# Performance work log

Hardware: AMD Instinct MI355X
Metric: run time of the kernel (lower is better)

The kernel has to match this reference:

```python
import jax, jax.numpy as jnp
from jax import lax
import numpy as np

NUM_COEFF = 24      # solver.num_coeff_per_dim (Chebyshev coefficients)
NUM_POINTS = 48     # Chebyshev-Gauss collocation nodes per interval
PICARD_ITERS = 5    # fixed-point iterations of the spectral PAN solve


def _cheb_setup(dtype):
    j = jnp.arange(NUM_POINTS, dtype=dtype)
    n = jnp.arange(NUM_COEFF, dtype=dtype)
    # tau_j = cos(pi*(j+1/2)/P); T[n, j] = T_n(tau_j) = cos(n*arccos(tau_j))
    ang = jnp.pi * (j + 0.5) / NUM_POINTS
    T = jnp.cos(n[:, None] * ang[None, :])                  # [C, P]
    V = (2.0 / NUM_POINTS) * T
    V = V.at[0].mul(0.5)                                    # DCT: a_n = sum_j f(tau_j) V[n, j]
    signs = jnp.cos(n * jnp.pi)                             # T_n(-1) = (-1)^n
    return T, V, signs


def _cheb_antiderivative(a, signs):
    # Chebyshev coeffs of int_{-1}^{tau} f, given coeffs a of f: b_n = (a_{n-1}-a_{n+1})/(2n)
    C = a.shape[-1]
    a_pad = jnp.concatenate([a, jnp.zeros_like(a[..., :2])], axis=-1)
    n = jnp.arange(1, C, dtype=a.dtype)
    b_rest = (a_pad[..., 0:C - 1] - a_pad[..., 2:C + 1]) / (2.0 * n)
    b0 = -jnp.sum(b_rest * signs[1:], axis=-1, keepdims=True)  # enforce value 0 at tau=-1
    return jnp.concatenate([b0, b_rest], axis=-1)


def _vf(y, W1, b1, W2, b2):
    # neural vector field f(t, y): autonomous MLP
    return jnp.tanh(y @ W1 + b1) @ W2 + b2


def _pan_solve(y_init, t_span, W1, b1, W2, b2):
    # Chebyshev-spectral (PAN) ODE solve; returns trajectory at t_span points
    # and the per-interval coefficient tensors B_all [I, batch, dim, C]
    T, V, signs = _cheb_setup(y_init.dtype)

    def solve_interval(y0, ts):
        t0, t1 = ts[0], ts[1]
        scale = (t1 - t0) * 0.5                             # dtau -> dt Jacobian

        def picard(B, _):
            y_nodes = jnp.einsum('bdc,cp->pbd', B, T)       # y at collocation nodes
            fvals = _vf(y_nodes, W1, b1, W2, b2)            # [P, batch, dim]
            a = jnp.einsum('pbd,cp->bdc', fvals, V)         # Chebyshev coeffs of f
            Bn = scale * _cheb_antiderivative(a, signs)
            Bn = Bn.at[..., 0].add(y0)                      # y(tau=-1) = y0
            return Bn, None

        B0 = jnp.zeros((*y0.shape, NUM_COEFF), y0.dtype).at[..., 0].set(y0)
        B, _ = lax.scan(picard, B0, None, length=PICARD_ITERS)
        y1 = jnp.sum(B, axis=-1)                            # T_n(1) = 1
        return y1, (B, y1)

    ts = jnp.stack([t_span[:-1], t_span[1:]], axis=-1)      # [I, 2]
    _, (B_all, y_ends) = lax.scan(solve_interval, y_init, ts)
    traj = jnp.concatenate([y_init[None], y_ends], axis=0)  # [I+1, batch, dim]
    return traj, B_all


def setup_inputs() -> dict:
    key = jax.random.key(0)
    k1, k2, k3 = jax.random.split(key, 3)
    batch, dim, hidden = 256, 512, 512
    s = np.float32(1.0 / np.sqrt(dim))
    return {
        'y_init': jax.random.normal(k1, (batch, dim), jnp.float32),
        't_span': jnp.linspace(0.0, 1.0, 7, dtype=jnp.float32),
        'W1': s * jax.random.normal(k2, (dim, hidden), jnp.float32),
        'b1': jnp.zeros((hidden,), jnp.float32),
        'W2': s * jax.random.normal(k3, (hidden, dim), jnp.float32),
        'b2': jnp.zeros((dim,), jnp.float32),
    }


def reference(y_init, t_span, W1, b1, W2, b2):
    traj, _B_all = _pan_solve(y_init, t_span, W1, b1, W2, b2)
    return (t_span, traj)
```

## Files before the change

### kernel.cpp

```cpp
#include <hip/hip_runtime.h>
#include <hip/hip_bf16.h>
#include <math.h>

#define NC 24
#define NP 48
#define NI 6
#define BATCH 256
#define DIM 512
#define NELEM (BATCH*DIM)
#define PROWS (BATCH*NC)

typedef __bf16 bf16x8 __attribute__((ext_vector_type(8)));
typedef unsigned short u16x8 __attribute__((ext_vector_type(8)));
typedef float f32x4 __attribute__((ext_vector_type(4)));
using bf16 = __hip_bfloat16;

struct bq8 { __hip_bfloat162 a, b; };

__device__ __forceinline__ void gld_lds16(const void* g, void* l) {
  __builtin_amdgcn_global_load_lds(
      (const __attribute__((address_space(1))) void*)g,
      (__attribute__((address_space(3))) void*)l, 16, 0, 0);
}

__device__ __forceinline__ float fast_tanh(float x) {
  float u = __expf(2.0f * x);
  float r = __builtin_amdgcn_rcpf(u + 1.0f);
  return __builtin_fmaf(-2.0f, r, 1.0f);
}

__device__ __forceinline__ float bfu(unsigned short u) {
  union { unsigned int i; float f; } v; v.i = ((unsigned)u) << 16; return v.f;
}

__global__ __launch_bounds__(256) void k_prep1(
    const float* __restrict__ t_span, const float* __restrict__ W1,
    const float* __restrict__ W2, const float* __restrict__ b1,
    const float* __restrict__ b2, const float* __restrict__ y_init,
    bf16* __restrict__ Tbf, bf16* __restrict__ Abf, float* __restrict__ a1,
    float* __restrict__ rs, float* __restrict__ wv, float* __restrict__ scales,
    float* __restrict__ zbias, float* __restrict__ out,
    bf16* __restrict__ W1T, bf16* __restrict__ W2T, bf16* __restrict__ W2bf,
    float* __restrict__ bb, float* __restrict__ y0, bf16* __restrict__ y0bf) {
  int bid = blockIdx.x;
  int tid = threadIdx.x;
  if (bid < 1024) {
    int idx = bid*256 + tid;
    int k = idx >> 9, n = idx & 511;
    W1T[n*DIM + k] = __float2bfloat16(W1[idx]);
    W2T[n*DIM + k] = __float2bfloat16(W2[idx]);
    W2bf[idx]      = __float2bfloat16(W2[idx]);
  } else if (bid < 1536) {
    int i = (bid - 1024)*256 + tid;
    float v = y_init[i];
    y0[i] = v; out[7 + i] = v;
    y0bf[i] = __float2bfloat16(v);
  } else if (bid < 1538) {
    int h = (bid - 1536)*256 + tid;
    float s = 0.f;
    for (int d = 0; d < DIM; d++) s = fmaf(b2[d], W1[d*DIM + h], s);
    bb[h] = s;
  } else {
    __shared__ double Tsh[NC][NP];
    __shared__ double Ashd[NC][NP];
    __shared__ double a1sh[NC];
    __shared__ double wsh[NP];
    for (int idx = tid; idx < NC*NP; idx += 256) {
      int c = idx / NP, p = idx % NP;
      Tsh[c][p] = cos((double)c * (M_PI * ((double)p + 0.5) / NP));
    }
    for (int idx = tid; idx < 32*64; idx += 256) Abf[idx] = __float2bfloat16(0.f);
    for (int idx = tid; idx < 48*32; idx += 256) Tbf[idx] = __float2bfloat16(0.f);
    __syncthreads();
    if (tid < NP) {
      int q = tid;
      double V[NC], K[NC];
      for (int c = 0; c < NC; c++) V[c] = (2.0/NP) * Tsh[c][q];
      V[0] *= 0.5;
      double s = 0.0;
      for (int n = 1; n < NC; n++) {
        double hi = (n+1 < NC) ? V[n+1] : 0.0;
        K[n] = (V[n-1] - hi) / (2.0*n);
        s += (n & 1) ? -K[n] : K[n];
      }
      K[0] = -s;
      double wsum = 0.0;
      for (int c = 0; c < NC; c++) wsum += K[c];
      wv[q] = (float)wsum;
      wsh[q] = wsum;
      for (int c = 0; c < NC; c++) {
        Ashd[c][q] = K[c];
        Abf[c*64 + q] = __float2bfloat16((float)K[c]);
      }
    }
    __syncthreads();
    if (tid < NC) {
      double s = 0.0;
      for (int q = 0; q < NP; q++) s += Ashd[tid][q];
      a1sh[tid] = s;
      a1[tid] = (float)s;
    }
    __syncthreads();
    if (tid < NP) {
      int p = tid;
      double r = 0.0;
      for (int c = 0; c < NC; c++) r += Tsh[c][p] * a1sh[c];
      rs[p] = (float)r;
      for (int c = 0; c < NC; c++) Tbf[p*32 + c] = __float2bfloat16((float)Tsh[c][p]);
    }
    if (tid == 0) {
      double s = 0.0;
      for (int q = 0; q < NP; q++) s += wsh[q];
      scales[6] = (float)s;
    }
    for (int idx = tid; idx < DIM; idx += 256) zbias[idx] = 0.f;
    if (tid < NI) scales[tid] = 0.5f*(t_span[tid+1]-t_span[tid]);
    if (tid < NI+1) out[tid] = t_span[tid];
  }
}

template<int EPI>
__device__ __forceinline__ void gemm_body(int vbid, int vgrid,
    bf16 (*sA)[128*64], bf16 (*sB)[64*64],
    const bf16* __restrict__ A, const bf16* __restrict__ BT,
    const float* __restrict__ bias, bf16* __restrict__ outb,
    float* __restrict__ outf) {
  int tid = threadIdx.x;
  int lane = tid & 63, wid = tid >> 6;
  int q8 = vgrid >> 3;
  int tl = (vbid & 7)*q8 + (vbid >> 3);
  int bm = tl >> 3, bn = tl & 7;
  int row0 = bm*128, col0 = bn*64;
  int wr = wid >> 1, wc = wid & 1;
  int r16 = lane & 15, g = lane >> 4;

  f32x4 acc[4][2];
  #pragma unroll
  for (int m = 0; m < 4; m++)
    #pragma unroll
    for (int n = 0; n < 2; n++)
      acc[m][n] = {0.f, 0.f, 0.f, 0.f};

  auto stage = [&](int buf, int k0) {
    #pragma unroll
    for (int j = 0; j < 4; j++) {
      int cid = wid*64 + lane + j*256;
      int r = cid >> 3;
      int c = (cid & 7) ^ (r & 7);
      gld_lds16(A + (size_t)(row0 + r)*DIM + k0 + c*8,
                (char*)&sA[buf][0] + wid*1024 + j*4096);
    }
    #pragma unroll
    for (int j = 0; j < 2; j++) {
      int cid = wid*64 + lane + j*256;
      int r = cid >> 3;
      int c = (cid & 7) ^ (r & 7);
      gld_lds16(BT + (size_t)(col0 + r)*DIM + k0 + c*8,
                (char*)&sB[buf][0] + wid*1024 + j*4096);
    }
  };

  stage(0, 0);
  int cur = 0;
  for (int k0 = 0; k0 < DIM; k0 += 64) {
    if (k0 + 64 < DIM) {
      stage(cur ^ 1, k0 + 64);
      asm volatile("s_waitcnt vmcnt(6)" ::: "memory");
    } else {
      asm volatile("s_waitcnt vmcnt(0)" ::: "memory");
    }
    __builtin_amdgcn_s_barrier();
    #pragma unroll
    for (int kk = 0; kk < 2; kk++) {
      bf16x8 af[4], bfr[2];
      #pragma unroll
      for (int m = 0; m < 4; m++) {
        int r = wr*64 + m*16 + r16;
        af[m] = *(const bf16x8*)(&sA[cur][0] + r*64 + (((kk*4+g) ^ (r&7))*8));
      }
      #pragma unroll
      for (int n = 0; n < 2; n++) {
        int r = wc*32 + n*16 + r16;
        bfr[n] = *(const bf16x8*)(&sB[cur][0] + r*64 + (((kk*4+g) ^ (r&7))*8));
      }
      #pragma unroll
      for (int m = 0; m < 4; m++)
        #pragma unroll
        for (int n = 0; n < 2; n++)
          acc[m][n] = __builtin_amdgcn_mfma_f32_16x16x32_bf16(af[m], bfr[n], acc[m][n], 0, 0, 0);
    }
    __builtin_amdgcn_s_barrier();
    cur ^= 1;
  }

  #pragma unroll
  for (int m = 0; m < 4; m++) {
    int rowb = row0 + wr*64 + m*16 + g*4;
    #pragma unroll
    for (int n = 0; n < 2; n++) {
      int col = col0 + wc*32 + n*16 + r16;
      float bv = bias[col];
      #pragma unroll
      for (int r = 0; r < 4; r++) {
        float v = acc[m][n][r] + bv;
        size_t idx = (size_t)(rowb + r)*DIM + col;
        if constexpr (EPI == 1) {
          outb[idx] = __float2bfloat16(v);
        } else {
          outf[idx] = v;
          outb[idx] = __float2bfloat16(fast_tanh(v));
        }
      }
    }
  }
}

__global__ __launch_bounds__(256, 3) void k_prep2(
    const bf16* __restrict__ W1T, const bf16* __restrict__ W2bf,
    const float* __restrict__ zbias, bf16* __restrict__ W21T,
    const bf16* __restrict__ y0bf, const float* __restrict__ b1,
    bf16* __restrict__ H1, float* __restrict__ C) {
  __shared__ bf16 sA[2][128*64];
  __shared__ bf16 sB[2][64*64];
  if (blockIdx.x < 32)
    gemm_body<1>(blockIdx.x, 32, sA, sB, W1T, W2bf, zbias, W21T, nullptr);
  else
    gemm_body<2>(blockIdx.x - 32, 16, sA, sB, y0bf, W1T, b1, H1, C);
}

template<int MODE>
__global__ __launch_bounds__(256, 2) void k_iter(
    const bf16* __restrict__ Pin, const bf16* __restrict__ H1,
    const bf16* __restrict__ W21T, const float* __restrict__ Cg,
    const float* __restrict__ bbg, const bf16* __restrict__ Tbf,
    const bf16* __restrict__ Abf, const float* __restrict__ a1,
    const float* __restrict__ rsg, const float* __restrict__ wvg,
    const float* __restrict__ scales, int t, bf16* __restrict__ outp) {
  __shared__ char smem[49152];
  int tid = threadIdx.x;
  int lane = tid & 63, wid = tid >> 6;
  int r16 = lane & 15, g = lane >> 4;
  int q8 = gridDim.x >> 3;
  int tl = (blockIdx.x & 7)*q8 + (blockIdx.x >> 3);
  int bm = tl >> 2, bn = tl & 3;
  int col0 = bn*128;
  int bglob0 = bm*2;

  if constexpr (MODE != 0) {
    int row0 = bm*48;
    f32x4 acc[3][2];
    #pragma unroll
    for (int m = 0; m < 3; m++)
      #pragma unroll
      for (int n = 0; n < 2; n++)
        acc[m][n] = {0.f, 0.f, 0.f, 0.f};

    auto stage = [&](int buf, int k0) {
      #pragma unroll
      for (int j = 0; j < 2; j++) {
        if (lane < 48) {
          int cid = j*192 + wid*48 + lane;
          int r = cid >> 3, cc = (cid & 7) ^ (r & 7);
          gld_lds16(Pin + (size_t)(row0 + r)*DIM + k0 + cc*8,
                    smem + buf*6144 + j*3072 + wid*768);
        }
      }
      #pragma unroll
      for (int j = 0; j < 4; j++) {
        int cid = j*256 + wid*64 + lane;
        int r = cid >> 3, cc = (cid & 7) ^ (r & 7);
        gld_lds16(W21T + (size_t)(col0 + r)*DIM + k0 + cc*8,
                  smem + 12288 + buf*16384 + j*4096 + wid*1024);
      }
    };

    stage(0, 0);
    int cur = 0;
    for (int ks = 0; ks < 8; ks++) {
      if (ks < 7) {
        stage(cur ^ 1, (ks+1)*64);
        asm volatile("s_waitcnt vmcnt(6)" ::: "memory");
      } else {
        asm volatile("s_waitcnt vmcnt(0)" ::: "memory");
      }
      __builtin_amdgcn_s_barrier();
      const char* sAc = smem + cur*6144;
      const char* sBc = smem + 12288 + cur*16384;
      #pragma unroll
      for (int kk = 0; kk < 2; kk++) {
        bf16x8 af[3], bfr[2];
        #pragma unroll
        for (int m = 0; m < 3; m++) {
          int r = m*16 + r16;
          af[m] = *(const bf16x8*)(sAc + r*128 + ((kk*4+g) ^ (r&7))*16);
        }
        #pragma unroll
        for (int n = 0; n < 2; n++) {
          int r = wid*32 + n*16 + r16;
          bfr[n] = *(const bf16x8*)(sBc + r*128 + ((kk*4+g) ^ (r&7))*16);
        }
        #pragma unroll
        for (int m = 0; m < 3; m++)
          #pragma unroll
          for (int n = 0; n < 2; n++)
            acc[m][n] = __builtin_amdgcn_mfma_f32_16x16x32_bf16(af[m], bfr[n], acc[m][n], 0, 0, 0);
      }
      __builtin_amdgcn_s_barrier();
      cur ^= 1;
    }

    #pragma unroll
    for (int m = 0; m < 3; m++) {
      int rowf = m*16 + g*4;
      int b_loc = rowf >= 24 ? 1 : 0;
      int c0 = rowf - b_loc*24;
      int slot = c0 >> 3;
      int inb  = (c0*2) & 15;
      #pragma unroll
      for (int n = 0; n < 2; n++) {
        int h = wid*32 + n*16 + r16;
        char* ad = smem + b_loc*8192 + h*64 + (((slot ^ ((h>>1)&3)) << 4) | inb);
        bq8 v;
        v.a = __hip_bfloat162{__float2bfloat16(acc[m][n][0]), __float2bfloat16(acc[m][n][1])};
        v.b = __hip_bfloat162{__float2bfloat16(acc[m][n][2]), __float2bfloat16(acc[m][n][3])};
        *(bq8*)ad = v;
      }
    }
  } else {
    bf16* sH1 = (bf16*)(smem + 16384);
    #pragma unroll
    for (int j = 0; j < 4; j++) {
      int e = j*256 + tid;
      int b = e >> 9, k = e & 511;
      sH1[e] = H1[(size_t)(bglob0 + b)*DIM + k];
    }
    __syncthreads();
    int b = tid >> 7, hl = tid & 127;
    int hg = col0 + hl;
    const bf16* wrow = W21T + (size_t)hg*DIM;
    const bf16* hrow = sH1 + b*512;
    float g1 = 0.f;
    for (int ks = 0; ks < 64; ks++) {
      u16x8 w8 = *(const u16x8*)(wrow + ks*8);
      u16x8 h8 = *(const u16x8*)(hrow + ks*8);
      #pragma unroll
      for (int i = 0; i < 8; i++)
        g1 = fmaf(bfu(h8[i]), bfu(w8[i]), g1);
    }
    __syncthreads();
    int rot = ((hl>>1)&3) << 4;
    #pragma unroll
    for (int c = 0; c < NC; c++) {
      int lb = c*2;
      char* ad = smem + b*8192 + hl*64 + ((( (lb>>4) << 4) ^ rot) | (lb & 15));
      *(bf16*)ad = __float2bfloat16(a1[c]*g1);
    }
  }

  if (tid < 256) {
    int bz = tid >> 7, hz = tid & 127;
    *(f32x4*)(smem + bz*8192 + hz*64 + ((3 ^ ((hz>>1)&3)) << 4)) = f32x4{0.f,0.f,0.f,0.f};
  }
  __syncthreads();

  int b_w = wid >> 1;
  int h0 = (wid & 1) << 6;
  int bglob = bglob0 + b_w;
  float sc = scales[t];

  f32x4 acc2[3][4];
  #pragma unroll
  for (int pt = 0; pt < 3; pt++)
    #pragma unroll
    for (int n2 = 0; n2 < 4; n2++)
      acc2[pt][n2] = {0.f, 0.f, 0.f, 0.f};
  {
    bf16x8 afT[3];
    #pragma unroll
    for (int pt = 0; pt < 3; pt++)
      afT[pt] = *(const bf16x8*)(Tbf + (pt*16 + r16)*32 + g*8);
    #pragma unroll
    for (int n2 = 0; n2 < 4; n2++) {
      int h = h0 + n2*16 + r16;
      bf16x8 b8 = *(const bf16x8*)(smem + b_w*8192 + h*64 + ((g ^ ((h>>1)&3)) << 4));
      #pragma unroll
      for (int pt = 0; pt < 3; pt++)
        acc2[pt][n2] = __builtin_amdgcn_mfma_f32_16x16x32_bf16(afT[pt], b8, acc2[pt][n2], 0, 0, 0);
    }
  }

  float rsv[12];
  #pragma unroll
  for (int pt = 0; pt < 3; pt++)
    #pragma unroll
    for (int r = 0; r < 4; r++)
      rsv[pt*4+r] = rsg[pt*16 + g*4 + r];

  if constexpr (MODE == 2) {
    float wvv[12];
    #pragma unroll
    for (int pt = 0; pt < 3; pt++)
      #pragma unroll
      for (int r = 0; r < 4; r++)
        wvv[pt*4+r] = wvg[pt*16 + g*4 + r];
    #pragma unroll
    for (int n2 = 0; n2 < 4; n2++) {
      int hg2 = col0 + h0 + n2*16 + r16;
      float cv = Cg[(size_t)bglob*DIM + hg2];
      float bbv = bbg[hg2];
      float hw = 0.f;
      #pragma unroll
      for (int pt = 0; pt < 3; pt++)
        #pragma unroll
        for (int r = 0; r < 4; r++) {
          float z = fmaf(sc, fmaf(rsv[pt*4+r], bbv, acc2[pt][n2][r]), cv);
          hw = fmaf(wvv[pt*4+r], fast_tanh(z), hw);
        }
      hw += __shfl_xor(hw, 16);
      hw += __shfl_xor(hw, 32);
      if (g == 0)
        outp[(size_t)bglob*DIM + hg2] = __float2bfloat16(hw);
    }
    return;
  } else {
    #pragma unroll
    for (int n2 = 0; n2 < 4; n2++) {
      int h = h0 + n2*16 + r16;
      int hg2 = col0 + h;
      float cv = Cg[(size_t)bglob*DIM + hg2];
      float bbv = bbg[hg2];
      #pragma unroll
      for (int pt = 0; pt < 3; pt++) {
        int p0 = pt*16 + g*4;
        float th[4];
        #pragma unroll
        for (int r = 0; r < 4; r++) {
          float z = fmaf(sc, fmaf(rsv[pt*4+r], bbv, acc2[pt][n2][r]), cv);
          th[r] = fast_tanh(z);
        }
        char* ad = smem + 16384 + b_w*16384 + h*128 + ((p0*2) ^ ((h&7)<<4));
        bq8 v;
        v.a = __hip_bfloat162{__float2bfloat16(th[0]), __float2bfloat16(th[1])};
        v.b = __hip_bfloat162{__float2bfloat16(th[2]), __float2bfloat16(th[3])};
        *(bq8*)ad = v;
      }
    }
    if (tid < 256) {
      int bz = tid >> 7, hz = tid & 127;
      char* base = smem + 16384 + bz*16384 + hz*128;
      *(f32x4*)(base + (96  ^ ((hz&7)<<4))) = f32x4{0.f,0.f,0.f,0.f};
      *(f32x4*)(base + (112 ^ ((hz&7)<<4))) = f32x4{0.f,0.f,0.f,0.f};
    }
    __syncthreads();

    f32x4 acc3[2][4];
    #pragma unroll
    for (int ct = 0; ct < 2; ct++)
      #pragma unroll
      for (int n2 = 0; n2 < 4; n2++)
        acc3[ct][n2] = {0.f, 0.f, 0.f, 0.f};
    bf16x8 afA[2][2];
    #pragma unroll
    for (int ct = 0; ct < 2; ct++)
      #pragma unroll
      for (int kk = 0; kk < 2; kk++)
        afA[ct][kk] = *(const bf16x8*)(Abf + (ct*16 + r16)*64 + kk*32 + g*8);
    #pragma unroll
    for (int kk = 0; kk < 2; kk++) {
      #pragma unroll
      for (int n2 = 0; n2 < 4; n2++) {
        int h = h0 + n2*16 + r16;
        bf16x8 b8 = *(const bf16x8*)(smem + 16384 + b_w*16384 + h*128 +
                                     ((kk*64 + g*16) ^ ((h&7)<<4)));
        #pragma unroll
        for (int ct = 0; ct < 2; ct++)
          acc3[ct][n2] = __builtin_amdgcn_mfma_f32_16x16x32_bf16(afA[ct][kk], b8, acc3[ct][n2], 0, 0, 0);
      }
    }
    #pragma unroll
    for (int n2 = 0; n2 < 4; n2++) {
      int hg2 = col0 + h0 + n2*16 + r16;
      #pragma unroll
      for (int ct = 0; ct < 2; ct++) {
        if (ct == 1 && g >= 2) continue;
        #pragma unroll
        for (int r = 0; r < 4; r++) {
          int c = ct*16 + g*4 + r;
          outp[((size_t)(bglob*NC + c))*DIM + hg2] = __float2bfloat16(acc3[ct][n2][r]);
        }
      }
    }
  }
}

__global__ __launch_bounds__(256, 3) void k_next(const bf16* __restrict__ A,
    const bf16* __restrict__ W2T, const bf16* __restrict__ W21T,
    const float* __restrict__ b2, const float* __restrict__ bb,
    float* __restrict__ y0, bf16* __restrict__ y0bf, float* __restrict__ C,
    bf16* __restrict__ H1, const float* __restrict__ scales, int t,
    float* __restrict__ traj) {
  __shared__ bf16 sA[2][128*64];
  __shared__ bf16 sB[2][64*64];
  int tid = threadIdx.x;
  int lane = tid & 63, wid = tid >> 6;
  int q8 = gridDim.x >> 3;
  int tl = (blockIdx.x & 7)*q8 + (blockIdx.x >> 3);
  int bm = tl >> 4, bn = tl & 15;
  int half = bn >> 3;
  int row0 = bm*128, col0 = (bn & 7)*64;
  const bf16* BT = half ? W21T : W2T;
  int wr = wid >> 1, wc = wid & 1;
  int r16 = lane & 15, g = lane >> 4;

  f32x4 acc[4][2];
  #pragma unroll
  for (int m = 0; m < 4; m++)
    #pragma unroll
    for (int n = 0; n < 2; n++)
      acc[m][n] = {0.f, 0.f, 0.f, 0.f};

  auto stage = [&](int buf, int k0) {
    #pragma unroll
    for (int j = 0; j < 4; j++) {
      int cid = wid*64 + lane + j*256;
      int r = cid >> 3;
      int c = (cid & 7) ^ (r & 7);
      gld_lds16(A + (size_t)(row0 + r)*DIM + k0 + c*8,
                (char*)&sA[buf][0] + wid*1024 + j*4096);
    }
    #pragma unroll
    for (int j = 0; j < 2; j++) {
      int cid = wid*64 + lane + j*256;
      int r = cid >> 3;
      int c = (cid & 7) ^ (r & 7);
      gld_lds16(BT + (size_t)(col0 + r)*DIM + k0 + c*8,
                (char*)&sB[buf][0] + wid*1024 + j*4096);
    }
  };

  stage(0, 0);
  int cur = 0;
  for (int k0 = 0; k0 < DIM; k0 += 64) {
    if (k0 + 64 < DIM) {
      stage(cur ^ 1, k0 + 64);
      asm volatile("s_waitcnt vmcnt(6)" ::: "memory");
    } else {
      asm volatile("s_waitcnt vmcnt(0)" ::: "memory");
    }
    __builtin_amdgcn_s_barrier();
    #pragma unroll
    for (int kk = 0; kk < 2; kk++) {
      bf16x8 af[4], bfr[2];
      #pragma unroll
      for (int m = 0; m < 4; m++) {
        int r = wr*64 + m*16 + r16;
        af[m] = *(const bf16x8*)(&sA[cur][0] + r*64 + (((kk*4+g) ^ (r&7))*8));
      }
      #pragma unroll
      for (int n = 0; n < 2; n++) {
        int r = wc*32 + n*16 + r16;
        bfr[n] = *(const bf16x8*)(&sB[cur][0] + r*64 + (((kk*4+g) ^ (r&7))*8));
      }
      #pragma unroll
      for (int m = 0; m < 4; m++)
        #pragma unroll
        for (int n = 0; n < 2; n++)
          acc[m][n] = __builtin_amdgcn_mfma_f32_16x16x32_bf16(af[m], bfr[n], acc[m][n], 0, 0, 0);
    }
    __builtin_amdgcn_s_barrier();
    cur ^= 1;
  }

  float sc = scales[t];
  float sumw = scales[6];
  #pragma unroll
  for (int m = 0; m < 4; m++) {
    int rowb = row0 + wr*64 + m*16 + g*4;
    #pragma unroll
    for (int n = 0; n < 2; n++) {
      int col = col0 + wc*32 + n*16 + r16;
      #pragma unroll
      for (int r = 0; r < 4; r++) {
        size_t idx = (size_t)(rowb + r)*DIM + col;
        if (half == 0) {
          float bv = sumw * b2[col];
          float y1 = fmaf(sc, acc[m][n][r] + bv, y0[idx]);
          y0[idx] = y1;
          y0bf[idx] = __float2bfloat16(y1);
          traj[idx] = y1;
        } else {
          float cb = sc * sumw * bb[col];
          float cnew = fmaf(sc, acc[m][n][r], C[idx] + cb);
          C[idx] = cnew;
          H1[idx] = __float2bfloat16(fast_tanh(cnew));
        }
      }
    }
  }
}

extern "C" void kernel_launch(void* const* d_in, const int* in_sizes, int n_in,
                              void* d_out, int out_size, void* d_ws, size_t ws_size,
                              hipStream_t stream) {
  const float* y_init = (const float*)d_in[0];
  const float* t_span = (const float*)d_in[1];
  const float* W1 = (const float*)d_in[2];
  const float* b1 = (const float*)d_in[3];
  const float* W2 = (const float*)d_in[4];
  const float* b2 = (const float*)d_in[5];
  float* out = (float*)d_out;

  char* ws = (char*)d_ws;
  size_t off = 0;
  auto carve = [&](size_t bytes) {
    void* p = ws + off; off += (bytes + 255) & ~(size_t)255; return p;
  };
  bf16*  Tbf    = (bf16*) carve((size_t)48*32*2);
  bf16*  Abf    = (bf16*) carve((size_t)32*64*2);
  float* a1     = (float*)carve(NC*4);
  float* rs     = (float*)carve(NP*4);
  float* wv     = (float*)carve(NP*4);
  float* bb     = (float*)carve(DIM*4);
  float* scales = (float*)carve(8*4);
  float* zbias  = (float*)carve(DIM*4);
  float* y0     = (float*)carve((size_t)NELEM*4);
  float* C      = (float*)carve((size_t)NELEM*4);
  bf16*  y0bf   = (bf16*) carve((size_t)NELEM*2);
  bf16*  H1     = (bf16*) carve((size_t)NELEM*2);
  bf16*  Hw     = (bf16*) carve((size_t)NELEM*2);
  bf16*  W1T    = (bf16*) carve((size_t)DIM*DIM*2);
  bf16*  W2T    = (bf16*) carve((size_t)DIM*DIM*2);
  bf16*  W2bf   = (bf16*) carve((size_t)DIM*DIM*2);
  bf16*  W21T   = (bf16*) carve((size_t)DIM*DIM*2);
  bf16*  Pa     = (bf16*) carve((size_t)PROWS*DIM*2);
  bf16*  Pb     = (bf16*) carve((size_t)PROWS*DIM*2);

  k_prep1<<<1539, 256, 0, stream>>>(t_span, W1, W2, b1, b2, y_init,
      Tbf, Abf, a1, rs, wv, scales, zbias, out, W1T, W2T, W2bf, bb, y0, y0bf);
  k_prep2<<<48, 256, 0, stream>>>(W1T, W2bf, zbias, W21T, y0bf, b1, H1, C);

  const int GRID = (BATCH/2)*(DIM/128);

  for (int t = 0; t < NI; t++) {
    k_iter<0><<<GRID, 256, 0, stream>>>(nullptr, H1, W21T, C, bb, Tbf, Abf,
                                        a1, rs, wv, scales, t, Pa);
    k_iter<1><<<GRID, 256, 0, stream>>>(Pa, nullptr, W21T, C, bb, Tbf, Abf,
                                        a1, rs, wv, scales, t, Pb);
    k_iter<1><<<GRID, 256, 0, stream>>>(Pb, nullptr, W21T, C, bb, Tbf, Abf,
                                        a1, rs, wv, scales, t, Pa);
    k_iter<2><<<GRID, 256, 0, stream>>>(Pa, nullptr, W21T, C, bb, Tbf, Abf,
                                        a1, rs, wv, scales, t, Hw);
    k_next<<<32, 256, 0, stream>>>(Hw, W2T, W21T, b2, bb, y0, y0bf, C, H1,
                                   scales, t, out + 7 + (size_t)(t+1)*NELEM);
  }
}
```

Measured before the change: 393.1 us.

## Fuse four Picard iteration kernels into one per-batch-row persistent kernel

Replaces the four k_iter launches per interval with a single k_pic kernel where each block owns one batch row and keeps the Chebyshev coefficient matrix P in LDS across all Picard iterations. This removes the global round-trips of the Pa/Pb intermediates and three launches per interval. The price is that every block re-streams the whole W21T matrix from global/L2 for each iteration, the kernel uses 112KB of dynamic LDS with 512 threads, and the grid shrinks to 256 blocks, which lowers occupancy.

Measured after the change: 480.1 us. +22.1%, slower.

```diff
diff --git a/kernel.cpp b/kernel.cpp
--- a/kernel.cpp
+++ b/kernel.cpp
@@ -8,7 +8,6 @@
 #define BATCH 256
 #define DIM 512
 #define NELEM (BATCH*DIM)
-#define PROWS (BATCH*NC)
 
 typedef __bf16 bf16x8 __attribute__((ext_vector_type(8)));
 typedef unsigned short u16x8 __attribute__((ext_vector_type(8)));
@@ -228,269 +227,219 @@
     gemm_body<2>(blockIdx.x - 32, 16, sA, sB, y0bf, W1T, b1, H1, C);
 }
 
-template<int MODE>
-__global__ __launch_bounds__(256, 2) void k_iter(
-    const bf16* __restrict__ Pin, const bf16* __restrict__ H1,
-    const bf16* __restrict__ W21T, const float* __restrict__ Cg,
-    const float* __restrict__ bbg, const bf16* __restrict__ Tbf,
-    const bf16* __restrict__ Abf, const float* __restrict__ a1,
-    const float* __restrict__ rsg, const float* __restrict__ wvg,
-    const float* __restrict__ scales, int t, bf16* __restrict__ outp) {
-  __shared__ char smem[49152];
+__global__ __launch_bounds__(512, 2) void k_pic(
+    const bf16* __restrict__ H1, const bf16* __restrict__ W21T,
+    const float* __restrict__ Cg, const float* __restrict__ bbg,
+    const bf16* __restrict__ Tbf, const bf16* __restrict__ Abf,
+    const float* __restrict__ a1g, const float* __restrict__ rsg,
+    const float* __restrict__ wvg, const float* __restrict__ scales, int t,
+    bf16* __restrict__ Hw) {
+  extern __shared__ char smem[];
+  char* P   = smem;
+  char* sGT = smem + 32768;
+  char* sHT = smem + 65536;
+  char* sB  = smem + 81920;
+  bf16* sH1 = (bf16*)(smem + 81920);
+
   int tid = threadIdx.x;
   int lane = tid & 63, wid = tid >> 6;
   int r16 = lane & 15, g = lane >> 4;
-  int q8 = gridDim.x >> 3;
-  int tl = (blockIdx.x & 7)*q8 + (blockIdx.x >> 3);
-  int bm = tl >> 2, bn = tl & 3;
-  int col0 = bn*128;
-  int bglob0 = bm*2;
-
-  if constexpr (MODE != 0) {
-    int row0 = bm*48;
-    f32x4 acc[3][2];
-    #pragma unroll
-    for (int m = 0; m < 3; m++)
-      #pragma unroll
-      for (int n = 0; n < 2; n++)
-        acc[m][n] = {0.f, 0.f, 0.f, 0.f};
-
-    auto stage = [&](int buf, int k0) {
-      #pragma unroll
-      for (int j = 0; j < 2; j++) {
-        if (lane < 48) {
-          int cid = j*192 + wid*48 + lane;
-          int r = cid >> 3, cc = (cid & 7) ^ (r & 7);
-          gld_lds16(Pin + (size_t)(row0 + r)*DIM + k0 + cc*8,
-                    smem + buf*6144 + j*3072 + wid*768);
-        }
-      }
-      #pragma unroll
-      for (int j = 0; j < 4; j++) {
-        int cid = j*256 + wid*64 + lane;
-        int r = cid >> 3, cc = (cid & 7) ^ (r & 7);
-        gld_lds16(W21T + (size_t)(col0 + r)*DIM + k0 + cc*8,
-                  smem + 12288 + buf*16384 + j*4096 + wid*1024);
-      }
-    };
-
-    stage(0, 0);
-    int cur = 0;
-    for (int ks = 0; ks < 8; ks++) {
-      if (ks < 7) {
-        stage(cur ^ 1, (ks+1)*64);
-        asm volatile("s_waitcnt vmcnt(6)" ::: "memory");
-      } else {
-        asm volatile("s_waitcnt vmcnt(0)" ::: "memory");
-      }
-      __builtin_amdgcn_s_barrier();
-      const char* sAc = smem + cur*6144;
-      const char* sBc = smem + 12288 + cur*16384;
-      #pragma unroll
-      for (int kk = 0; kk < 2; kk++) {
-        bf16x8 af[3], bfr[2];
-        #pragma unroll
-        for (int m = 0; m < 3; m++) {
-          int r = m*16 + r16;
-          af[m] = *(const bf16x8*)(sAc + r*128 + ((kk*4+g) ^ (r&7))*16);
-        }
-        #pragma unroll
-        for (int n = 0; n < 2; n++) {
-          int r = wid*32 + n*16 + r16;
-          bfr[n] = *(const bf16x8*)(sBc + r*128 + ((kk*4+g) ^ (r&7))*16);
-        }
-        #pragma unroll
-        for (int m = 0; m < 3; m++)
-          #pragma unroll
-          for (int n = 0; n < 2; n++)
-            acc[m][n] = __builtin_amdgcn_mfma_f32_16x16x32_bf16(af[m], bfr[n], acc[m][n], 0, 0, 0);
-      }
-      __builtin_amdgcn_s_barrier();
-      cur ^= 1;
-    }
-
-    #pragma unroll
-    for (int m = 0; m < 3; m++) {
-      int rowf = m*16 + g*4;
-      int b_loc = rowf >= 24 ? 1 : 0;
-      int c0 = rowf - b_loc*24;
-      int slot = c0 >> 3;
-      int inb  = (c0*2) & 15;
-      #pragma unroll
-      for (int n = 0; n < 2; n++) {
-        int h = wid*32 + n*16 + r16;
-        char* ad = smem + b_loc*8192 + h*64 + (((slot ^ ((h>>1)&3)) << 4) | inb);
-        bq8 v;
-        v.a = __hip_bfloat162{__float2bfloat16(acc[m][n][0]), __float2bfloat16(acc[m][n][1])};
-        v.b = __hip_bfloat162{__float2bfloat16(acc[m][n][2]), __float2bfloat16(acc[m][n][3])};
-        *(bq8*)ad = v;
-      }
-    }
-  } else {
-    bf16* sH1 = (bf16*)(smem + 16384);
-    #pragma unroll
-    for (int j = 0; j < 4; j++) {
-      int e = j*256 + tid;
-      int b = e >> 9, k = e & 511;
-      sH1[e] = H1[(size_t)(bglob0 + b)*DIM + k];
-    }
-    __syncthreads();
-    int b = tid >> 7, hl = tid & 127;
-    int hg = col0 + hl;
-    const bf16* wrow = W21T + (size_t)hg*DIM;
-    const bf16* hrow = sH1 + b*512;
+  int b = ((int)blockIdx.x & 7)*32 + ((int)blockIdx.x >> 3);
+  float sc = scales[t];
+
+  bf16x8 afT[3];
+  #pragma unroll
+  for (int pt = 0; pt < 3; pt++)
+    afT[pt] = *(const bf16x8*)(Tbf + (pt*16 + r16)*32 + g*8);
+  bf16x8 afA[2][2];
+  #pragma unroll
+  for (int ct = 0; ct < 2; ct++)
+    #pragma unroll
+    for (int kk = 0; kk < 2; kk++)
+      afA[ct][kk] = *(const bf16x8*)(Abf + (ct*16 + r16)*64 + kk*32 + g*8);
+  float rsv[12], wvv[12];
+  #pragma unroll
+  for (int pt = 0; pt < 3; pt++)
+    #pragma unroll
+    for (int r = 0; r < 4; r++) {
+      rsv[pt*4+r] = rsg[pt*16 + g*4 + r];
+      wvv[pt*4+r] = wvg[pt*16 + g*4 + r];
+    }
+  float cv[4], bbv[4];
+  #pragma unroll
+  for (int tile = 0; tile < 4; tile++) {
+    int hG = tile*128 + wid*16 + r16;
+    cv[tile]  = Cg[(size_t)b*DIM + hG];
+    bbv[tile] = bbg[hG];
+  }
+
+  *(f32x4*)(P + 24*1024 + tid*16) = f32x4{0.f,0.f,0.f,0.f};
+  sH1[tid] = H1[(size_t)b*DIM + tid];
+  __syncthreads();
+
+  {
+    int h = tid;
+    const bf16* wrow = W21T + (size_t)h*DIM;
     float g1 = 0.f;
     for (int ks = 0; ks < 64; ks++) {
       u16x8 w8 = *(const u16x8*)(wrow + ks*8);
-      u16x8 h8 = *(const u16x8*)(hrow + ks*8);
+      u16x8 h8 = *(const u16x8*)(sH1 + ks*8);
       #pragma unroll
       for (int i = 0; i < 8; i++)
         g1 = fmaf(bfu(h8[i]), bfu(w8[i]), g1);
     }
-    __syncthreads();
-    int rot = ((hl>>1)&3) << 4;
+    int rot = ((h>>1)&3) << 4;
     #pragma unroll
     for (int c = 0; c < NC; c++) {
       int lb = c*2;
-      char* ad = smem + b*8192 + hl*64 + ((( (lb>>4) << 4) ^ rot) | (lb & 15));
-      *(bf16*)ad = __float2bfloat16(a1[c]*g1);
-    }
-  }
-
-  if (tid < 256) {
-    int bz = tid >> 7, hz = tid & 127;
-    *(f32x4*)(smem + bz*8192 + hz*64 + ((3 ^ ((hz>>1)&3)) << 4)) = f32x4{0.f,0.f,0.f,0.f};
+      *(bf16*)(sGT + h*64 + ((((lb>>4)<<4) ^ rot) | (lb & 15))) =
+          __float2bfloat16(a1g[c]*g1);
+    }
+    *(f32x4*)(sGT + h*64 + ((3<<4) ^ rot)) = f32x4{0.f,0.f,0.f,0.f};
   }
   __syncthreads();
 
-  int b_w = wid >> 1;
-  int h0 = (wid & 1) << 6;
-  int bglob = bglob0 + b_w;
-  float sc = scales[t];
-
-  f32x4 acc2[3][4];
-  #pragma unroll
-  for (int pt = 0; pt < 3; pt++)
-    #pragma unroll
-    for (int n2 = 0; n2 < 4; n2++)
-      acc2[pt][n2] = {0.f, 0.f, 0.f, 0.f};
-  {
-    bf16x8 afT[3];
-    #pragma unroll
-    for (int pt = 0; pt < 3; pt++)
-      afT[pt] = *(const bf16x8*)(Tbf + (pt*16 + r16)*32 + g*8);
-    #pragma unroll
-    for (int n2 = 0; n2 < 4; n2++) {
-      int h = h0 + n2*16 + r16;
-      bf16x8 b8 = *(const bf16x8*)(smem + b_w*8192 + h*64 + ((g ^ ((h>>1)&3)) << 4));
-      #pragma unroll
-      for (int pt = 0; pt < 3; pt++)
-        acc2[pt][n2] = __builtin_amdgcn_mfma_f32_16x16x32_bf16(afT[pt], b8, acc2[pt][n2], 0, 0, 0);
-    }
-  }
-
-  float rsv[12];
-  #pragma unroll
-  for (int pt = 0; pt < 3; pt++)
-    #pragma unroll
-    for (int r = 0; r < 4; r++)
-      rsv[pt*4+r] = rsg[pt*16 + g*4 + r];
-
-  if constexpr (MODE == 2) {
-    float wvv[12];
-    #pragma unroll
-    for (int pt = 0; pt < 3; pt++)
-      #pragma unroll
-      for (int r = 0; r < 4; r++)
-        wvv[pt*4+r] = wvg[pt*16 + g*4 + r];
-    #pragma unroll
-    for (int n2 = 0; n2 < 4; n2++) {
-      int hg2 = col0 + h0 + n2*16 + r16;
-      float cv = Cg[(size_t)bglob*DIM + hg2];
-      float bbv = bbg[hg2];
-      float hw = 0.f;
-      #pragma unroll
-      for (int pt = 0; pt < 3; pt++)
-        #pragma unroll
-        for (int r = 0; r < 4; r++) {
-          float z = fmaf(sc, fmaf(rsv[pt*4+r], bbv, acc2[pt][n2][r]), cv);
-          hw = fmaf(wvv[pt*4+r], fast_tanh(z), hw);
-        }
-      hw += __shfl_xor(hw, 16);
-      hw += __shfl_xor(hw, 32);
-      if (g == 0)
-        outp[(size_t)bglob*DIM + hg2] = __float2bfloat16(hw);
-    }
-    return;
-  } else {
-    #pragma unroll
-    for (int n2 = 0; n2 < 4; n2++) {
-      int h = h0 + n2*16 + r16;
-      int hg2 = col0 + h;
-      float cv = Cg[(size_t)bglob*DIM + hg2];
-      float bbv = bbg[hg2];
-      #pragma unroll
-      for (int pt = 0; pt < 3; pt++) {
-        int p0 = pt*16 + g*4;
-        float th[4];
-        #pragma unroll
-        for (int r = 0; r < 4; r++) {
-          float z = fmaf(sc, fmaf(rsv[pt*4+r], bbv, acc2[pt][n2][r]), cv);
-          th[r] = fast_tanh(z);
-        }
-        char* ad = smem + 16384 + b_w*16384 + h*128 + ((p0*2) ^ ((h&7)<<4));
-        bq8 v;
-        v.a = __hip_bfloat162{__float2bfloat16(th[0]), __float2bfloat16(th[1])};
-        v.b = __hip_bfloat162{__float2bfloat16(th[2]), __float2bfloat16(th[3])};
-        *(bq8*)ad = v;
-      }
-    }
-    if (tid < 256) {
-      int bz = tid >> 7, hz = tid & 127;
-      char* base = smem + 16384 + bz*16384 + hz*128;
-      *(f32x4*)(base + (96  ^ ((hz&7)<<4))) = f32x4{0.f,0.f,0.f,0.f};
-      *(f32x4*)(base + (112 ^ ((hz&7)<<4))) = f32x4{0.f,0.f,0.f,0.f};
-    }
-    __syncthreads();
-
-    f32x4 acc3[2][4];
-    #pragma unroll
-    for (int ct = 0; ct < 2; ct++)
-      #pragma unroll
-      for (int n2 = 0; n2 < 4; n2++)
-        acc3[ct][n2] = {0.f, 0.f, 0.f, 0.f};
-    bf16x8 afA[2][2];
-    #pragma unroll
-    for (int ct = 0; ct < 2; ct++)
-      #pragma unroll
-      for (int kk = 0; kk < 2; kk++)
-        afA[ct][kk] = *(const bf16x8*)(Abf + (ct*16 + r16)*64 + kk*32 + g*8);
-    #pragma unroll
-    for (int kk = 0; kk < 2; kk++) {
-      #pragma unroll
-      for (int n2 = 0; n2 < 4; n2++) {
-        int h = h0 + n2*16 + r16;
-        bf16x8 b8 = *(const bf16x8*)(smem + 16384 + b_w*16384 + h*128 +
-                                     ((kk*64 + g*16) ^ ((h&7)<<4)));
-        #pragma unroll
-        for (int ct = 0; ct < 2; ct++)
-          acc3[ct][n2] = __builtin_amdgcn_mfma_f32_16x16x32_bf16(afA[ct][kk], b8, acc3[ct][n2], 0, 0, 0);
-      }
-    }
-    #pragma unroll
-    for (int n2 = 0; n2 < 4; n2++) {
-      int hg2 = col0 + h0 + n2*16 + r16;
-      #pragma unroll
-      for (int ct = 0; ct < 2; ct++) {
-        if (ct == 1 && g >= 2) continue;
-        #pragma unroll
-        for (int r = 0; r < 4; r++) {
-          int c = ct*16 + g*4 + r;
-          outp[((size_t)(bglob*NC + c))*DIM + hg2] = __float2bfloat16(acc3[ct][n2][r]);
-        }
-      }
-    }
-  }
+  auto phaseA = [&]() {
+    int mrow = (wid >> 2)*16, nc0 = (wid & 3)*32;
+    f32x4 acc[2];
+    acc[0] = f32x4{0.f,0.f,0.f,0.f}; acc[1] = f32x4{0.f,0.f,0.f,0.f};
+    auto stage = [&](int s) {
+      int col0 = (s >> 3)*128, k0 = (s & 7)*64;
+      int buf = s & 1;
+      #pragma unroll
+      for (int j = 0; j < 2; j++) {
+        int cid = j*512 + tid;
+        int r = cid >> 3, cc = (cid & 7) ^ (r & 7);
+        gld_lds16(W21T + (size_t)(col0 + r)*DIM + k0 + cc*8,
+                  sB + buf*16384 + j*8192 + wid*1024);
+      }
+    };
+    stage(0);
+    for (int s = 0; s < 32; s++) {
+      if (s < 31) {
+        stage(s+1);
+        asm volatile("s_waitcnt vmcnt(2)" ::: "memory");
+      } else {
+        asm volatile("s_waitcnt vmcnt(0)" ::: "memory");
+      }
+      __builtin_amdgcn_s_barrier();
+      const char* sBc = sB + (s & 1)*16384;
+      int k0 = (s & 7)*64;
+      #pragma unroll
+      for (int kk = 0; kk < 2; kk++) {
+        int rA = mrow + r16;
+        bf16x8 af = *(const bf16x8*)(P + rA*1024 +
+                     (((k0 + kk*32 + g*8)*2) ^ ((rA&7)<<4)));
+        bf16x8 bfr[2];
+        #pragma unroll
+        for (int n = 0; n < 2; n++) {
+          int rB = nc0 + n*16 + r16;
+          bfr[n] = *(const bf16x8*)(sBc + rB*128 + ((kk*4+g) ^ (rB&7))*16);
+        }
+        #pragma unroll
+        for (int n = 0; n < 2; n++)
+          acc[n] = __builtin_amdgcn_mfma_f32_16x16x32_bf16(af, bfr[n], acc[n], 0, 0, 0);
+      }
+      if ((s & 7) == 7) {
+        int tile = s >> 3;
+        int c0 = mrow + g*4;
+        int slot = c0 >> 3, inb = (c0*2) & 15;
+        #pragma unroll
+        for (int n = 0; n < 2; n++) {
+          int h = tile*128 + nc0 + n*16 + r16;
+          char* ad = sGT + h*64 + (((slot ^ ((h>>1)&3)) << 4) | inb);
+          bq8 v;
+          v.a = __hip_bfloat162{__float2bfloat16(acc[n][0]), __float2bfloat16(acc[n][1])};
+          v.b = __hip_bfloat162{__float2bfloat16(acc[n][2]), __float2bfloat16(acc[n][3])};
+          *(bq8*)ad = v;
+        }
+        acc[0] = f32x4{0.f,0.f,0.f,0.f}; acc[1] = f32x4{0.f,0.f,0.f,0.f};
+      }
+      __builtin_amdgcn_s_barrier();
+    }
+  };
+
+  auto phaseBC = [&](bool fin) {
+    #pragma unroll
+    for (int tile = 0; tile < 4; tile++) {
+      int h_loc = wid*16 + r16;
+      int hG = tile*128 + h_loc;
+      f32x4 acc2[3];
+      #pragma unroll
+      for (int pt = 0; pt < 3; pt++) acc2[pt] = f32x4{0.f,0.f,0.f,0.f};
+      {
+        bf16x8 bfr = *(const bf16x8*)(sGT + hG*64 + ((g ^ ((hG>>1)&3)) << 4));
+        #pragma unroll
+        for (int pt = 0; pt < 3; pt++)
+          acc2[pt] = __builtin_amdgcn_mfma_f32_16x16x32_bf16(afT[pt], bfr, acc2[pt], 0, 0, 0);
+      }
+      if (fin) {
+        float hw = 0.f;
+        #pragma unroll
+        for (int pt = 0; pt < 3; pt++)
+          #pragma unroll
+          for (int r = 0; r < 4; r++) {
+            float z = fmaf(sc, fmaf(rsv[pt*4+r], bbv[tile], acc2[pt][r]), cv[tile]);
+            hw = fmaf(wvv[pt*4+r], fast_tanh(z), hw);
+          }
+        hw += __shfl_xor(hw, 16);
+        hw += __shfl_xor(hw, 32);
+        if (g == 0)
+          Hw[(size_t)b*DIM + hG] = __float2bfloat16(hw);
+      } else {
+        #pragma unroll
+        for (int pt = 0; pt < 3; pt++) {
+          int p0 = pt*16 + g*4;
+          float th[4];
+          #pragma unroll
+          for (int r = 0; r < 4; r++) {
+            float z = fmaf(sc, fmaf(rsv[pt*4+r], bbv[tile], acc2[pt][r]), cv[tile]);
+            th[r] = fast_tanh(z);
+          }
+          char* ad = sHT + h_loc*128 + ((p0*2) ^ ((h_loc&7)<<4));
+          bq8 v;
+          v.a = __hip_bfloat162{__float2bfloat16(th[0]), __float2bfloat16(th[1])};
+          v.b = __hip_bfloat162{__float2bfloat16(th[2]), __float2bfloat16(th[3])};
+          *(bq8*)ad = v;
+        }
+        if (tid < 128) {
+          char* base = sHT + tid*128;
+          *(f32x4*)(base + (96  ^ ((tid&7)<<4))) = f32x4{0.f,0.f,0.f,0.f};
+          *(f32x4*)(base + (112 ^ ((tid&7)<<4))) = f32x4{0.f,0.f,0.f,0.f};
+        }
+        __syncthreads();
+        f32x4 acc3[2];
+        acc3[0] = f32x4{0.f,0.f,0.f,0.f}; acc3[1] = f32x4{0.f,0.f,0.f,0.f};
+        #pragma unroll
+        for (int kk = 0; kk < 2; kk++) {
+          bf16x8 b8 = *(const bf16x8*)(sHT + h_loc*128 +
+                       ((kk*64 + g*16) ^ ((h_loc&7)<<4)));
+          #pragma unroll
+          for (int ct = 0; ct < 2; ct++)
+            acc3[ct] = __builtin_amdgcn_mfma_f32_16x16x32_bf16(afA[ct][kk], b8, acc3[ct], 0, 0, 0);
+        }
+        #pragma unroll
+        for (int ct = 0; ct < 2; ct++) {
+          if (ct == 1 && g >= 2) continue;
+          #pragma unroll
+          for (int r = 0; r < 4; r++) {
+            int c = ct*16 + g*4 + r;
+            *(bf16*)(P + c*1024 + ((hG*2) ^ ((c&7)<<4))) =
+                __float2bfloat16(acc3[ct][r]);
+          }
+        }
+        __syncthreads();
+      }
+    }
+  };
+
+  phaseBC(false);
+  phaseA(); __syncthreads();
+  phaseBC(false);
+  phaseA(); __syncthreads();
+  phaseBC(false);
+  phaseA(); __syncthreads();
+  phaseBC(true);
 }
 
 __global__ __launch_bounds__(256, 3) void k_next(const bf16* __restrict__ A,
@@ -632,24 +581,18 @@
   bf16*  W2T    = (bf16*) carve((size_t)DIM*DIM*2);
   bf16*  W2bf   = (bf16*) carve((size_t)DIM*DIM*2);
   bf16*  W21T   = (bf16*) carve((size_t)DIM*DIM*2);
-  bf16*  Pa     = (bf16*) carve((size_t)PROWS*DIM*2);
-  bf16*  Pb     = (bf16*) carve((size_t)PROWS*DIM*2);
+
+  const int PIC_LDS = 114688;
+  hipFuncSetAttribute(reinterpret_cast<const void*>(&k_pic),
+                      hipFuncAttributeMaxDynamicSharedMemorySize, PIC_LDS);
 
   k_prep1<<<1539, 256, 0, stream>>>(t_span, W1, W2, b1, b2, y_init,
       Tbf, Abf, a1, rs, wv, scales, zbias, out, W1T, W2T, W2bf, bb, y0, y0bf);
   k_prep2<<<48, 256, 0, stream>>>(W1T, W2bf, zbias, W21T, y0bf, b1, H1, C);
 
-  const int GRID = (BATCH/2)*(DIM/128);
-
   for (int t = 0; t < NI; t++) {
-    k_iter<0><<<GRID, 256, 0, stream>>>(nullptr, H1, W21T, C, bb, Tbf, Abf,
-                                        a1, rs, wv, scales, t, Pa);
-    k_iter<1><<<GRID, 256, 0, stream>>>(Pa, nullptr, W21T, C, bb, Tbf, Abf,
-                                        a1, rs, wv, scales, t, Pb);
-    k_iter<1><<<GRID, 256, 0, stream>>>(Pb, nullptr, W21T, C, bb, Tbf, Abf,
-                                        a1, rs, wv, scales, t, Pa);
-    k_iter<2><<<GRID, 256, 0, stream>>>(Pa, nullptr, W21T, C, bb, Tbf, Abf,
-                                        a1, rs, wv, scales, t, Hw);
+    k_pic<<<BATCH, 512, PIC_LDS, stream>>>(H1, W21T, C, bb, Tbf, Abf,
+                                           a1, rs, wv, scales, t, Hw);
     k_next<<<32, 256, 0, stream>>>(Hw, W2T, W21T, b2, bb, y0, y0bf, C, H1,
                                    scales, t, out + 7 + (size_t)(t+1)*NELEM);
   }
```
